# Kernel optimization log

Measured on AMD Instinct MI355X. Metric: run time of the kernel, lower is better.

The kernel has to match this reference:

```python
import jax, jax.numpy as jnp
import numpy as np

N_HEAD, F_IN, F_OUT = 4, 768, 64
BS, N = 4, 2048


def setup_inputs() -> dict:
    key = jax.random.key(0)
    k_h, k_w, k_src, k_dst = jax.random.split(key, 4)
    # xavier_uniform bounds
    lim_w = float(np.sqrt(6.0 / (F_IN + F_OUT)))
    lim_a = float(np.sqrt(6.0 / (F_OUT + 1)))
    return {
        "h": jax.random.normal(k_h, (BS, N, F_IN), dtype=jnp.float32),
        "w": jax.random.uniform(k_w, (N_HEAD, F_IN, F_OUT), jnp.float32, -lim_w, lim_w),
        "a_src": jax.random.uniform(k_src, (N_HEAD, F_OUT, 1), jnp.float32, -lim_a, lim_a),
        "a_dst": jax.random.uniform(k_dst, (N_HEAD, F_OUT, 1), jnp.float32, -lim_a, lim_a),
        "bias": jnp.zeros((F_OUT,), dtype=jnp.float32),
    }


def reference(h, w, a_src, a_dst, bias):
    # h: [b, n, f_in]; w: [h, f_in, f_out]
    h_prime = jnp.einsum("bnf,hfo->bhno", h, w)          # [b, h, n, f_out]
    t = jnp.tanh(h_prime)
    attn_src = jnp.einsum("bhno,ho->bhn", t, a_src[..., 0])  # [b, h, n]
    attn_dst = jnp.einsum("bhno,ho->bhn", t, a_dst[..., 0])  # [b, h, n]
    # broadcast add: attn[b,h,i,j] = src[b,h,i] + dst[b,h,j]
    attn = attn_src[..., :, None] + attn_dst[..., None, :]   # [b, h, n, n]
    attn = jnp.where(attn >= 0, attn, 0.2 * attn)            # leaky_relu(0.2)
    attn = jax.nn.softmax(attn, axis=-1)
    out = jnp.einsum("bhij,bhjo->bhio", attn, h_prime)       # [b, h, n, f_out]
    return out + bias
```

## Files before the change

### kernel.cpp

```cpp
#include <hip/hip_runtime.h>
#include <hip/hip_bf16.h>

#define NHEAD 4
#define FIN   768
#define FOUT  64
#define BSZ   4
#define NSEQ  2048
#define BH    (BSZ*NHEAD)
#define LOG2E 1.44269504088896f

typedef __attribute__((ext_vector_type(8)))  short bf16x8;
typedef __attribute__((ext_vector_type(16))) float f32x16;
typedef __attribute__((ext_vector_type(8)))  unsigned short u16x8;
typedef __attribute__((ext_vector_type(4)))  unsigned short u16x4;
typedef __attribute__((ext_vector_type(4)))  unsigned u32x4;

__device__ __forceinline__ unsigned short f2bf(float f){
  unsigned b = __float_as_uint(f);
  return (unsigned short)((b + 0x7fffu + ((b >> 16) & 1u)) >> 16);
}
__device__ __forceinline__ float fexp2(float x){
#if __has_builtin(__builtin_amdgcn_exp2f)
  return __builtin_amdgcn_exp2f(x);
#else
  return exp2f(x);
#endif
}
__device__ __forceinline__ unsigned pkbf(float lo, float hi){
#if __has_builtin(__builtin_amdgcn_cvt_pk_bf16_f32)
  typedef __attribute__((ext_vector_type(2))) __bf16 bf2;
  union { bf2 v; unsigned u; } cv;
  cv.v = __builtin_amdgcn_cvt_pk_bf16_f32(lo, hi);
  return cv.u;
#else
  return (unsigned)f2bf(lo) | ((unsigned)f2bf(hi) << 16);
#endif
}

__global__ __launch_bounds__(512, 2) void k_hprime(
    const float* __restrict__ h, const float* __restrict__ w,
    const float* __restrict__ a_src, const float* __restrict__ a_dst,
    unsigned short* __restrict__ hpz2, float* __restrict__ srcv,
    float* __restrict__ dstv)
{
  __shared__ __align__(16) char smem[65536];
  float* psumS = (float*)(smem + 16384);
  float* psumD = (float*)(smem + 16896);
  char*  Tt    = smem + 32768;

  const int tid  = threadIdx.x;
  const int bid  = blockIdx.x;
  const int bh1  = (bid & 7) | (((bid >> 3) & 1) << 3);
  const int head = bh1 & 3;
  const int jbase = (bid >> 4) << 6;
  const int i0a   = (bh1 >> 2)*NSEQ + jbase;
  const int wave = tid >> 6, lane = tid & 63;
  const int wm = wave & 1, wn = (wave >> 1) & 1, kw = wave >> 2;
  const int l32 = lane & 31, h32 = lane >> 5;

  f32x16 acc = {0,0,0,0,0,0,0,0,0,0,0,0,0,0,0,0};

  const int sr = tid >> 3, sc = tid & 7;
  const float* hA = h + (size_t)(i0a + sr)*FIN + sc*8;
  const int aslot = (sc ^ (sr & 7)) << 4;

  const int ob = tid & 63, cc = tid >> 6;
  const float* wsrc = w + (size_t)head*FIN*FOUT + ob;
  const int bslot0 = ((cc & 7) ^ (ob & 7)) << 4;

  float4 ra0 = *(const float4*)(hA);
  float4 ra1 = *(const float4*)(hA + 4);
  float4 ra2 = *(const float4*)(hA + 64);
  float4 ra3 = *(const float4*)(hA + 68);
  float rb[16];
  #pragma unroll
  for (int j = 0; j < 8; ++j){
    rb[j]     = wsrc[(size_t)(cc*8 + j)*FOUT];
    rb[8 + j] = wsrc[(size_t)(64 + cc*8 + j)*FOUT];
  }

  for (int it = 0; it < 6; ++it){
    char* Ab = smem +         (it & 1)*16384;
    char* Bb = smem + 32768 + (it & 1)*16384;
    u32x4 pk0, pk1;
    pk0[0] = pkbf(ra0.x, ra0.y); pk0[1] = pkbf(ra0.z, ra0.w);
    pk0[2] = pkbf(ra1.x, ra1.y); pk0[3] = pkbf(ra1.z, ra1.w);
    pk1[0] = pkbf(ra2.x, ra2.y); pk1[1] = pkbf(ra2.z, ra2.w);
    pk1[2] = pkbf(ra3.x, ra3.y); pk1[3] = pkbf(ra3.z, ra3.w);
    *(u32x4*)(Ab + sr*256 + aslot)        = pk0;
    *(u32x4*)(Ab + sr*256 + 128 + aslot)  = pk1;
    u32x4 qb0, qb1;
    qb0[0] = pkbf(rb[0],  rb[1]);  qb0[1] = pkbf(rb[2],  rb[3]);
    qb0[2] = pkbf(rb[4],  rb[5]);  qb0[3] = pkbf(rb[6],  rb[7]);
    qb1[0] = pkbf(rb[8],  rb[9]);  qb1[1] = pkbf(rb[10], rb[11]);
    qb1[2] = pkbf(rb[12], rb[13]); qb1[3] = pkbf(rb[14], rb[15]);
    *(u32x4*)(Bb + ob*256 +       bslot0) = qb0;
    *(u32x4*)(Bb + ob*256 + 128 + bslot0) = qb1;
    __syncthreads();
    if (it < 5){
      const float* an = hA + (it+1)*128;
      ra0 = *(const float4*)(an);      ra1 = *(const float4*)(an + 4);
      ra2 = *(const float4*)(an + 64); ra3 = *(const float4*)(an + 68);
      const float* wn_ = wsrc + (size_t)(it+1)*128*FOUT;
      #pragma unroll
      for (int j = 0; j < 8; ++j){
        rb[j]     = wn_[(size_t)(cc*8 + j)*FOUT];
        rb[8 + j] = wn_[(size_t)(64 + cc*8 + j)*FOUT];
      }
    }
    #pragma unroll
    for (int s = 0; s < 4; ++s){
      const int slot = (((s*2 + h32) ^ (l32 & 7)) << 4);
      bf16x8 av = *(const bf16x8*)(Ab + (wm*32 + l32)*256 + kw*128 + slot);
      bf16x8 bv = *(const bf16x8*)(Bb + (wn*32 + l32)*256 + kw*128 + slot);
      acc = __builtin_amdgcn_mfma_f32_32x32x16_bf16(av, bv, acc, 0, 0, 0);
    }
  }

  if (kw == 1) *(f32x16*)(smem + (size_t)((wave & 3)*64 + lane)*64) = acc;
  __syncthreads();
  if (kw == 0){
    acc += *(const f32x16*)(smem + (size_t)((wave & 3)*64 + lane)*64);
    const float as = a_src[head*64 + wn*32 + l32];
    const float ad = a_dst[head*64 + wn*32 + l32];
    #pragma unroll
    for (int rb2 = 0; rb2 < 4; ++rb2){
      const int jb = wm*32 + rb2*8 + h32*4;
      u16x4 c4;
      #pragma unroll
      for (int q = 0; q < 4; ++q){
        const float v = acc[rb2*4 + q];
        c4[q] = f2bf(v);
        const float t = tanhf(v);
        float ps = t*as, pd = t*ad;
        ps += __shfl_xor(ps, 1);  ps += __shfl_xor(ps, 2);  ps += __shfl_xor(ps, 4);
        ps += __shfl_xor(ps, 8);  ps += __shfl_xor(ps, 16);
        pd += __shfl_xor(pd, 1);  pd += __shfl_xor(pd, 2);  pd += __shfl_xor(pd, 4);
        pd += __shfl_xor(pd, 8);  pd += __shfl_xor(pd, 16);
        if (l32 == 0){
          psumS[(jb + q)*2 + wn] = ps;
          psumD[(jb + q)*2 + wn] = pd;
        }
      }
      const int orow = wn*32 + l32;
      const int slot = ((jb >> 3) & 7) ^ (orow & 7);
      *(u16x4*)(Tt + orow*128 + slot*16 + (jb & 7)*2) = c4;
    }
  }
  __syncthreads();

  {
    const int o = tid & 63, c = tid >> 6;
    u16x8 val = *(const u16x8*)(Tt + o*128 + ((c ^ (o & 7)) << 4));
    *(u16x8*)((char*)hpz2 + ((size_t)(bh1*256 + (jbase >> 3) + c)*64 + o)*16) = val;
  }
  if (tid < 64){
    srcv[(size_t)bh1*NSEQ + jbase + tid] = (psumS[tid*2] + psumS[tid*2 + 1]) * LOG2E;
    dstv[(size_t)bh1*NSEQ + jbase + tid] = (psumD[tid*2] + psumD[tid*2 + 1]) * LOG2E;
  }
}

__global__ __launch_bounds__(512, 4) void k_attn(
    const unsigned short* __restrict__ hpz2, const float* __restrict__ srcv,
    const float* __restrict__ dstv, const float* __restrict__ bias,
    float* __restrict__ out)
{
  __shared__ __align__(16) char smem[33792];
  float* Lbuf = (float*)(smem + 32768);

  const int tid = threadIdx.x;
  const int bid = blockIdx.x;
  const int bh  = (bid & 7) | (((bid >> 3) & 1) << 3);
  const int i0  = (bid >> 4) << 6;
  const int wave = tid >> 6, lane = tid & 63;
  const int wm = wave & 1, jw = wave >> 1;
  const int l32 = lane & 31, h32 = lane >> 5;

  const float s2 = srcv[(size_t)bh*NSEQ + i0 + wm*32 + l32];
  const float u_ = s2;
  const float v_ = 0.2f*s2;
  const float* dptr = dstv + (size_t)bh*NSEQ;

  const u16x8* gp = (const u16x8*)((const char*)hpz2 + (size_t)bh*256*64*16);

  f32x16 accO0 = {0,0,0,0,0,0,0,0,0,0,0,0,0,0,0,0};
  f32x16 accO1 = {0,0,0,0,0,0,0,0,0,0,0,0,0,0,0,0};
  float lpart = 0.f;

  *(u16x8*)(smem + tid*16)         = gp[tid];
  *(u16x8*)(smem + (tid + 512)*16) = gp[tid + 512];
  __syncthreads();

  for (int w = 0; w < 16; ++w){
    char* cur = smem + (w & 1)*16384;
    char* nxt = smem + ((w + 1) & 1)*16384;
    u16x8 r0, r1;
    if (w < 15){
      r0 = gp[(w+1)*1024 + tid];
      r1 = gp[(w+1)*1024 + tid + 512];
    }
    #pragma unroll
    for (int stl = 0; stl < 2; ++stl){
      const int Jl = jw*4 + stl*2 + h32;
      const int j0 = (w*16 + Jl)*8;
      float4 d0 = *(const float4*)(dptr + j0);
      float4 d1 = *(const float4*)(dptr + j0 + 4);
      float e0,e1,e2,e3,e4,e5,e6,e7;
      e0 = fexp2(fmaxf(u_ + d0.x, fmaf(0.2f, d0.x, v_)));
      e1 = fexp2(fmaxf(u_ + d0.y, fmaf(0.2f, d0.y, v_)));
      e2 = fexp2(fmaxf(u_ + d0.z, fmaf(0.2f, d0.z, v_)));
      e3 = fexp2(fmaxf(u_ + d0.w, fmaf(0.2f, d0.w, v_)));
      e4 = fexp2(fmaxf(u_ + d1.x, fmaf(0.2f, d1.x, v_)));
      e5 = fexp2(fmaxf(u_ + d1.y, fmaf(0.2f, d1.y, v_)));
      e6 = fexp2(fmaxf(u_ + d1.z, fmaf(0.2f, d1.z, v_)));
      e7 = fexp2(fmaxf(u_ + d1.w, fmaf(0.2f, d1.w, v_)));
      lpart += ((e0+e1)+(e2+e3)) + ((e4+e5)+(e6+e7));
      u32x4 pk;
      pk[0] = pkbf(e0, e1); pk[1] = pkbf(e2, e3);
      pk[2] = pkbf(e4, e5); pk[3] = pkbf(e6, e7);
      const bf16x8 pA = __builtin_bit_cast(bf16x8, pk);
      const bf16x8 bv0 = *(const bf16x8*)(cur + (Jl*64 +      l32)*16);
      const bf16x8 bv1 = *(const bf16x8*)(cur + (Jl*64 + 32 + l32)*16);
      accO0 = __builtin_amdgcn_mfma_f32_32x32x16_bf16(pA, bv0, accO0, 0, 0, 0);
      accO1 = __builtin_amdgcn_mfma_f32_32x32x16_bf16(pA, bv1, accO1, 0, 0, 0);
    }
    if (w < 15){
      *(u16x8*)(nxt + tid*16)         = r0;
      *(u16x8*)(nxt + (tid + 512)*16) = r1;
    }
    __syncthreads();
  }

  lpart += __shfl_xor(lpart, 32);
  if (lane < 32) Lbuf[(wm*4 + jw)*32 + l32] = lpart;

  const float4 bia = *(const float4*)(bias + (tid & 15)*4);
  #pragma unroll
  for (int ph = 0; ph < 2; ++ph){
    __syncthreads();
    if (wm == ph){
      float* ob = (float*)smem;
      #pragma unroll
      for (int reg = 0; reg < 16; ++reg){
        const int m = (reg & 3) + 8*(reg >> 2) + 4*h32;
        ob[(jw*32 + m)*64 +      l32] = accO0[reg];
        ob[(jw*32 + m)*64 + 32 + l32] = accO1[reg];
      }
    }
    __syncthreads();
    {
      const int i = tid >> 4, o4 = (tid & 15)*4;
      const float* ob = (const float*)smem;
      float4 v0 = *(const float4*)(ob + (0*32 + i)*64 + o4);
      float4 v1 = *(const float4*)(ob + (1*32 + i)*64 + o4);
      float4 v2 = *(const float4*)(ob + (2*32 + i)*64 + o4);
      float4 v3 = *(const float4*)(ob + (3*32 + i)*64 + o4);
      const float l = Lbuf[(ph*4+0)*32 + i] + Lbuf[(ph*4+1)*32 + i]
                    + Lbuf[(ph*4+2)*32 + i] + Lbuf[(ph*4+3)*32 + i];
      const float r = 1.f / l;
      float4 res;
      res.x = (v0.x + v1.x + v2.x + v3.x)*r + bia.x;
      res.y = (v0.y + v1.y + v2.y + v3.y)*r + bia.y;
      res.z = (v0.z + v1.z + v2.z + v3.z)*r + bia.z;
      res.w = (v0.w + v1.w + v2.w + v3.w)*r + bia.w;
      *(float4*)(out + ((size_t)bh*NSEQ + i0 + ph*32 + i)*64 + o4) = res;
    }
  }
}

extern "C" void kernel_launch(void* const* d_in, const int* in_sizes, int n_in,
                              void* d_out, int out_size, void* d_ws, size_t ws_size,
                              hipStream_t stream)
{
  const float* h     = (const float*)d_in[0];
  const float* w     = (const float*)d_in[1];
  const float* a_src = (const float*)d_in[2];
  const float* a_dst = (const float*)d_in[3];
  const float* bias  = (const float*)d_in[4];
  float* out = (float*)d_out;

  char* ws = (char*)d_ws;
  unsigned short* hpz2 = (unsigned short*)ws;
  float* srcv = (float*)(ws + (4u<<20));
  float* dstv = (float*)(ws + (4u<<20) + (128u<<10));

  k_hprime<<<512, 512, 0, stream>>>(h, w, a_src, a_dst, hpz2, srcv, dstv);
  k_attn<<<512, 512, 0, stream>>>(hpz2, srcv, dstv, bias, out);
}
```

Measured before the change: 119.1 us.

## Pre-convert h and w to swizzled bf16 and stream tiles via global_load_lds

Adds a prep kernel that converts h and w to bf16 once, already laid out in the swizzled LDS order. The projection kernel then fills its double-buffered LDS tiles with direct global-to-LDS loads instead of register loads plus packing, and raises its occupancy hint. tanh becomes an exp2/rcp approximation. The aim is to halve operand bytes read in the GEMM and drop per-thread conversion work, at the cost of an extra launch and an extra full round trip of h through memory.

New measurement: 121.8 us. +2.3%, slower.

```diff
diff --git a/kernel.cpp b/kernel.cpp
--- a/kernel.cpp
+++ b/kernel.cpp
@@ -36,9 +36,56 @@
   return (unsigned)f2bf(lo) | ((unsigned)f2bf(hi) << 16);
 #endif
 }
-
-__global__ __launch_bounds__(512, 2) void k_hprime(
+__device__ __forceinline__ float fast_tanh(float v){
+  const float e = fexp2(v * (2.0f*LOG2E));
+#if __has_builtin(__builtin_amdgcn_rcpf)
+  return 1.0f - 2.0f*__builtin_amdgcn_rcpf(e + 1.0f);
+#else
+  return 1.0f - 2.0f/(e + 1.0f);
+#endif
+}
+__device__ __forceinline__ void gll16(const void* g, void* l){
+  __builtin_amdgcn_global_load_lds(
+      (const __attribute__((address_space(1))) unsigned*)g,
+      (__attribute__((address_space(3))) unsigned*)l, 16, 0, 0);
+}
+
+__global__ __launch_bounds__(512) void k_prep(
     const float* __restrict__ h, const float* __restrict__ w,
+    unsigned short* __restrict__ h_bf, unsigned short* __restrict__ w_bf)
+{
+  const int tid = threadIdx.x;
+  const int bid = blockIdx.x;
+  if (bid < 1536){
+    const int gid = bid*512 + tid;
+    const int row = gid / 96;
+    const int rem = gid - row*96;
+    const int it  = rem >> 4, p = rem & 15;
+    const float* src = h + (size_t)row*FIN + it*128 + ((p>>3)<<6)
+                         + (((p & 7) ^ (row & 7)) << 3);
+    const float4 a = *(const float4*)src;
+    const float4 b = *(const float4*)(src + 4);
+    u32x4 pk;
+    pk[0] = pkbf(a.x, a.y); pk[1] = pkbf(a.z, a.w);
+    pk[2] = pkbf(b.x, b.y); pk[3] = pkbf(b.z, b.w);
+    *(u32x4*)((char*)h_bf + (size_t)gid*16) = pk;
+  } else {
+    const int wid = (bid - 1536)*512 + tid;
+    const int p   = wid & 15, o = (wid >> 4) & 63, hi6 = wid >> 10;
+    const int head = hi6 / 6, it = hi6 - head*6;
+    const int k0 = it*128 + ((p>>3)<<6) + (((p & 7) ^ (o & 7)) << 3);
+    const float* sw = w + (size_t)head*FIN*FOUT + (size_t)k0*FOUT + o;
+    float r0 = sw[0*FOUT], r1 = sw[1*FOUT], r2 = sw[2*FOUT], r3 = sw[3*FOUT];
+    float r4 = sw[4*FOUT], r5 = sw[5*FOUT], r6 = sw[6*FOUT], r7 = sw[7*FOUT];
+    u32x4 pk;
+    pk[0] = pkbf(r0, r1); pk[1] = pkbf(r2, r3);
+    pk[2] = pkbf(r4, r5); pk[3] = pkbf(r6, r7);
+    *(u32x4*)((char*)w_bf + (size_t)wid*16) = pk;
+  }
+}
+
+__global__ __launch_bounds__(512, 4) void k_hprime(
+    const unsigned short* __restrict__ h_bf, const unsigned short* __restrict__ w_bf,
     const float* __restrict__ a_src, const float* __restrict__ a_dst,
     unsigned short* __restrict__ hpz2, float* __restrict__ srcv,
     float* __restrict__ dstv)
@@ -60,53 +107,34 @@
 
   f32x16 acc = {0,0,0,0,0,0,0,0,0,0,0,0,0,0,0,0};
 
-  const int sr = tid >> 3, sc = tid & 7;
-  const float* hA = h + (size_t)(i0a + sr)*FIN + sc*8;
-  const int aslot = (sc ^ (sr & 7)) << 4;
-
-  const int ob = tid & 63, cc = tid >> 6;
-  const float* wsrc = w + (size_t)head*FIN*FOUT + ob;
-  const int bslot0 = ((cc & 7) ^ (ob & 7)) << 4;
-
-  float4 ra0 = *(const float4*)(hA);
-  float4 ra1 = *(const float4*)(hA + 4);
-  float4 ra2 = *(const float4*)(hA + 64);
-  float4 ra3 = *(const float4*)(hA + 68);
-  float rb[16];
-  #pragma unroll
-  for (int j = 0; j < 8; ++j){
-    rb[j]     = wsrc[(size_t)(cc*8 + j)*FOUT];
-    rb[8 + j] = wsrc[(size_t)(64 + cc*8 + j)*FOUT];
-  }
+  const int rowL = wave*4 + (lane >> 4);
+  const int p16  = lane & 15;
+  const char* sA = (const char*)h_bf + ((size_t)(i0a + rowL)*96 + p16)*16;
+  const char* sB = (const char*)w_bf + (size_t)(head*6)*16384 + rowL*256 + p16*16;
+
+  {
+    char* AbW = smem +         wave*1024;
+    char* BbW = smem + 32768 + wave*1024;
+    gll16(sA,         AbW);
+    gll16(sA + 49152, AbW + 8192);
+    gll16(sB,         BbW);
+    gll16(sB + 8192,  BbW + 8192);
+  }
+  __syncthreads();
 
   for (int it = 0; it < 6; ++it){
-    char* Ab = smem +         (it & 1)*16384;
-    char* Bb = smem + 32768 + (it & 1)*16384;
-    u32x4 pk0, pk1;
-    pk0[0] = pkbf(ra0.x, ra0.y); pk0[1] = pkbf(ra0.z, ra0.w);
-    pk0[2] = pkbf(ra1.x, ra1.y); pk0[3] = pkbf(ra1.z, ra1.w);
-    pk1[0] = pkbf(ra2.x, ra2.y); pk1[1] = pkbf(ra2.z, ra2.w);
-    pk1[2] = pkbf(ra3.x, ra3.y); pk1[3] = pkbf(ra3.z, ra3.w);
-    *(u32x4*)(Ab + sr*256 + aslot)        = pk0;
-    *(u32x4*)(Ab + sr*256 + 128 + aslot)  = pk1;
-    u32x4 qb0, qb1;
-    qb0[0] = pkbf(rb[0],  rb[1]);  qb0[1] = pkbf(rb[2],  rb[3]);
-    qb0[2] = pkbf(rb[4],  rb[5]);  qb0[3] = pkbf(rb[6],  rb[7]);
-    qb1[0] = pkbf(rb[8],  rb[9]);  qb1[1] = pkbf(rb[10], rb[11]);
-    qb1[2] = pkbf(rb[12], rb[13]); qb1[3] = pkbf(rb[14], rb[15]);
-    *(u32x4*)(Bb + ob*256 +       bslot0) = qb0;
-    *(u32x4*)(Bb + ob*256 + 128 + bslot0) = qb1;
-    __syncthreads();
+    const int bb = it & 1;
+    char* Ab = smem +         bb*16384;
+    char* Bb = smem + 32768 + bb*16384;
     if (it < 5){
-      const float* an = hA + (it+1)*128;
-      ra0 = *(const float4*)(an);      ra1 = *(const float4*)(an + 4);
-      ra2 = *(const float4*)(an + 64); ra3 = *(const float4*)(an + 68);
-      const float* wn_ = wsrc + (size_t)(it+1)*128*FOUT;
-      #pragma unroll
-      for (int j = 0; j < 8; ++j){
-        rb[j]     = wn_[(size_t)(cc*8 + j)*FOUT];
-        rb[8 + j] = wn_[(size_t)(64 + cc*8 + j)*FOUT];
-      }
+      char* AbW = smem +         (bb^1)*16384 + wave*1024;
+      char* BbW = smem + 32768 + (bb^1)*16384 + wave*1024;
+      const char* sAi = sA + (size_t)(it+1)*256;
+      const char* sBi = sB + (size_t)(it+1)*16384;
+      gll16(sAi,         AbW);
+      gll16(sAi + 49152, AbW + 8192);
+      gll16(sBi,         BbW);
+      gll16(sBi + 8192,  BbW + 8192);
     }
     #pragma unroll
     for (int s = 0; s < 4; ++s){
@@ -115,6 +143,7 @@
       bf16x8 bv = *(const bf16x8*)(Bb + (wn*32 + l32)*256 + kw*128 + slot);
       acc = __builtin_amdgcn_mfma_f32_32x32x16_bf16(av, bv, acc, 0, 0, 0);
     }
+    __syncthreads();
   }
 
   if (kw == 1) *(f32x16*)(smem + (size_t)((wave & 3)*64 + lane)*64) = acc;
@@ -131,7 +160,7 @@
       for (int q = 0; q < 4; ++q){
         const float v = acc[rb2*4 + q];
         c4[q] = f2bf(v);
-        const float t = tanhf(v);
+        const float t = fast_tanh(v);
         float ps = t*as, pd = t*ad;
         ps += __shfl_xor(ps, 1);  ps += __shfl_xor(ps, 2);  ps += __shfl_xor(ps, 4);
         ps += __shfl_xor(ps, 8);  ps += __shfl_xor(ps, 16);
@@ -283,7 +312,10 @@
   unsigned short* hpz2 = (unsigned short*)ws;
   float* srcv = (float*)(ws + (4u<<20));
   float* dstv = (float*)(ws + (4u<<20) + (128u<<10));
-
-  k_hprime<<<512, 512, 0, stream>>>(h, w, a_src, a_dst, hpz2, srcv, dstv);
+  unsigned short* h_bf = (unsigned short*)(ws + (8u<<20));
+  unsigned short* w_bf = (unsigned short*)(ws + (8u<<20) + 12582912u);
+
+  k_prep<<<1584, 512, 0, stream>>>(h, w, h_bf, w_bf);
+  k_hprime<<<512, 512, 0, stream>>>(h_bf, w_bf, a_src, a_dst, hpz2, srcv, dstv);
   k_attn<<<512, 512, 0, stream>>>(hpz2, srcv, dstv, bias, out);
 }
```

## Load value tiles straight from global into registers, dropping LDS staging and barriers

Applied to the files above, without the earlier changes.

The main loop no longer stages the bf16 value tiles through double-buffered shared memory with a block barrier each step. Each lane now loads its own MFMA B operands directly from global memory into registers and prefetches the next step's operands while computing the current one. This removes the LDS writes, LDS reads and per-iteration __syncthreads. In exchange the global loads are less coalesced, each element is fetched from L2 by every wave that needs it, and more registers are used for prefetching.

New measurement: 115.7 us. 2.8% less time.

```diff
diff --git a/kernel.cpp b/kernel.cpp
--- a/kernel.cpp
+++ b/kernel.cpp
@@ -179,56 +179,63 @@
   const float s2 = srcv[(size_t)bh*NSEQ + i0 + wm*32 + l32];
   const float u_ = s2;
   const float v_ = 0.2f*s2;
-  const float* dptr = dstv + (size_t)bh*NSEQ;
 
   const u16x8* gp = (const u16x8*)((const char*)hpz2 + (size_t)bh*256*64*16);
+  const u16x8* tp = gp + ((jw*4 + h32)*64 + l32);
+  const float* dS = dstv + (size_t)bh*NSEQ + (jw*4 + h32)*8;
 
   f32x16 accO0 = {0,0,0,0,0,0,0,0,0,0,0,0,0,0,0,0};
   f32x16 accO1 = {0,0,0,0,0,0,0,0,0,0,0,0,0,0,0,0};
   float lpart = 0.f;
 
-  *(u16x8*)(smem + tid*16)         = gp[tid];
-  *(u16x8*)(smem + (tid + 512)*16) = gp[tid + 512];
-  __syncthreads();
+  u16x8 c0 = tp[0], c1 = tp[32], c2 = tp[128], c3 = tp[160];
 
   for (int w = 0; w < 16; ++w){
-    char* cur = smem + (w & 1)*16384;
-    char* nxt = smem + ((w + 1) & 1)*16384;
-    u16x8 r0, r1;
+    u16x8 n0, n1, n2, n3;
     if (w < 15){
-      r0 = gp[(w+1)*1024 + tid];
-      r1 = gp[(w+1)*1024 + tid + 512];
-    }
-    #pragma unroll
-    for (int stl = 0; stl < 2; ++stl){
-      const int Jl = jw*4 + stl*2 + h32;
-      const int j0 = (w*16 + Jl)*8;
-      float4 d0 = *(const float4*)(dptr + j0);
-      float4 d1 = *(const float4*)(dptr + j0 + 4);
-      float e0,e1,e2,e3,e4,e5,e6,e7;
-      e0 = fexp2(fmaxf(u_ + d0.x, fmaf(0.2f, d0.x, v_)));
-      e1 = fexp2(fmaxf(u_ + d0.y, fmaf(0.2f, d0.y, v_)));
-      e2 = fexp2(fmaxf(u_ + d0.z, fmaf(0.2f, d0.z, v_)));
-      e3 = fexp2(fmaxf(u_ + d0.w, fmaf(0.2f, d0.w, v_)));
-      e4 = fexp2(fmaxf(u_ + d1.x, fmaf(0.2f, d1.x, v_)));
-      e5 = fexp2(fmaxf(u_ + d1.y, fmaf(0.2f, d1.y, v_)));
-      e6 = fexp2(fmaxf(u_ + d1.z, fmaf(0.2f, d1.z, v_)));
-      e7 = fexp2(fmaxf(u_ + d1.w, fmaf(0.2f, d1.w, v_)));
+      const u16x8* np = tp + 1024;
+      n0 = np[0]; n1 = np[32]; n2 = np[128]; n3 = np[160];
+    }
+    float4 d0 = *(const float4*)(dS);
+    float4 d1 = *(const float4*)(dS + 4);
+    float4 d2 = *(const float4*)(dS + 16);
+    float4 d3 = *(const float4*)(dS + 20);
+    {
+      float e0 = fexp2(fmaxf(u_ + d0.x, fmaf(0.2f, d0.x, v_)));
+      float e1 = fexp2(fmaxf(u_ + d0.y, fmaf(0.2f, d0.y, v_)));
+      float e2 = fexp2(fmaxf(u_ + d0.z, fmaf(0.2f, d0.z, v_)));
+      float e3 = fexp2(fmaxf(u_ + d0.w, fmaf(0.2f, d0.w, v_)));
+      float e4 = fexp2(fmaxf(u_ + d1.x, fmaf(0.2f, d1.x, v_)));
+      float e5 = fexp2(fmaxf(u_ + d1.y, fmaf(0.2f, d1.y, v_)));
+      float e6 = fexp2(fmaxf(u_ + d1.z, fmaf(0.2f, d1.z, v_)));
+      float e7 = fexp2(fmaxf(u_ + d1.w, fmaf(0.2f, d1.w, v_)));
       lpart += ((e0+e1)+(e2+e3)) + ((e4+e5)+(e6+e7));
       u32x4 pk;
       pk[0] = pkbf(e0, e1); pk[1] = pkbf(e2, e3);
       pk[2] = pkbf(e4, e5); pk[3] = pkbf(e6, e7);
       const bf16x8 pA = __builtin_bit_cast(bf16x8, pk);
-      const bf16x8 bv0 = *(const bf16x8*)(cur + (Jl*64 +      l32)*16);
-      const bf16x8 bv1 = *(const bf16x8*)(cur + (Jl*64 + 32 + l32)*16);
-      accO0 = __builtin_amdgcn_mfma_f32_32x32x16_bf16(pA, bv0, accO0, 0, 0, 0);
-      accO1 = __builtin_amdgcn_mfma_f32_32x32x16_bf16(pA, bv1, accO1, 0, 0, 0);
-    }
-    if (w < 15){
-      *(u16x8*)(nxt + tid*16)         = r0;
-      *(u16x8*)(nxt + (tid + 512)*16) = r1;
-    }
-    __syncthreads();
+      accO0 = __builtin_amdgcn_mfma_f32_32x32x16_bf16(pA, c0, accO0, 0, 0, 0);
+      accO1 = __builtin_amdgcn_mfma_f32_32x32x16_bf16(pA, c1, accO1, 0, 0, 0);
+    }
+    {
+      float e0 = fexp2(fmaxf(u_ + d2.x, fmaf(0.2f, d2.x, v_)));
+      float e1 = fexp2(fmaxf(u_ + d2.y, fmaf(0.2f, d2.y, v_)));
+      float e2 = fexp2(fmaxf(u_ + d2.z, fmaf(0.2f, d2.z, v_)));
+      float e3 = fexp2(fmaxf(u_ + d2.w, fmaf(0.2f, d2.w, v_)));
+      float e4 = fexp2(fmaxf(u_ + d3.x, fmaf(0.2f, d3.x, v_)));
+      float e5 = fexp2(fmaxf(u_ + d3.y, fmaf(0.2f, d3.y, v_)));
+      float e6 = fexp2(fmaxf(u_ + d3.z, fmaf(0.2f, d3.z, v_)));
+      float e7 = fexp2(fmaxf(u_ + d3.w, fmaf(0.2f, d3.w, v_)));
+      lpart += ((e0+e1)+(e2+e3)) + ((e4+e5)+(e6+e7));
+      u32x4 pk;
+      pk[0] = pkbf(e0, e1); pk[1] = pkbf(e2, e3);
+      pk[2] = pkbf(e4, e5); pk[3] = pkbf(e6, e7);
+      const bf16x8 pA = __builtin_bit_cast(bf16x8, pk);
+      accO0 = __builtin_amdgcn_mfma_f32_32x32x16_bf16(pA, c2, accO0, 0, 0, 0);
+      accO1 = __builtin_amdgcn_mfma_f32_32x32x16_bf16(pA, c3, accO1, 0, 0, 0);
+    }
+    tp += 1024; dS += 128;
+    c0 = n0; c1 = n1; c2 = n2; c3 = n3;
   }
 
   lpart += __shfl_xor(lpart, 32);
```
